# Optimization experiments

Hardware: AMD Instinct MI355X
Metric: run time of the kernel (lower is better)

The kernel has to match this reference:

```python
import jax, jax.numpy as jnp
import numpy as np

N, L, D, H, DFF = 16, 192, 512, 8, 2048
HD = D // H


def _mha(q, k, v, wq, bq, wk, bk, wv, bv, wo, bo, mask=None):
    # q: [B, Lq, D], k/v: [B, Lk, D]
    B, Lq, _ = q.shape
    def proj(x, W, b):
        y = x @ W + b
        return y.reshape(B, -1, H, HD).transpose(0, 2, 1, 3)  # [B, H, L, HD]
    Q, K, V = proj(q, wq, bq), proj(k, wk, bk), proj(v, wv, bv)
    QK = jnp.einsum('bhqd,bhkd->bhqk', Q, K) / jnp.sqrt(jnp.asarray(HD, Q.dtype))
    if mask is not None:
        QK = QK + (1.0 - mask) * (-1e9)
    A = jax.nn.softmax(QK, axis=-1)
    out = jnp.einsum('bhqk,bhkd->bhqd', A, V).transpose(0, 2, 1, 3).reshape(B, Lq, D)
    return out @ wo + bo


def _ln(x, g, b, eps=1e-6):
    mu = x.mean(-1, keepdims=True)
    var = ((x - mu) ** 2).mean(-1, keepdims=True)
    return (x - mu) / jnp.sqrt(var + eps) * g + b


def setup_inputs() -> dict:
    key = jax.random.key(0)
    ks = jax.random.split(key, 16)
    w = lambda k, sh: jax.random.normal(k, sh, jnp.float32) * 0.02
    inp = {
        'S': jax.random.normal(ks[0], (N, L, D), jnp.float32),
        'padding_mask': jax.random.randint(ks[1], (N * N, 1, 1, L), 0, 2, dtype=jnp.int32),
        'training': 0,
    }
    for i, nm in enumerate(['ca_wq', 'ca_wk', 'ca_wv', 'ca_wo', 'ia_wq', 'ia_wk', 'ia_wv', 'ia_wo']):
        inp[nm] = w(ks[2 + i], (D, D))
        inp[nm.replace('w', 'b')] = jnp.zeros((D,), jnp.float32)
    inp['ffn_w1'] = w(ks[10], (D, DFF)); inp['ffn_b1'] = jnp.zeros((DFF,), jnp.float32)
    inp['ffn_w2'] = w(ks[11], (DFF, D)); inp['ffn_b2'] = jnp.zeros((D,), jnp.float32)
    inp['ln1_g'] = jnp.ones((D,), jnp.float32); inp['ln1_b'] = jnp.zeros((D,), jnp.float32)
    inp['ln2_g'] = jnp.ones((D,), jnp.float32); inp['ln2_b'] = jnp.zeros((D,), jnp.float32)
    return inp


def reference(S, ca_wq, ca_bq, ca_wk, ca_bk, ca_wv, ca_bv, ca_wo, ca_bo,
              ia_wq, ia_bq, ia_wk, ia_bk, ia_wv, ia_bv, ia_wo, ia_bo,
              ffn_w1, ffn_b1, ffn_w2, ffn_b2, ln1_g, ln1_b, ln2_g, ln2_b,
              padding_mask, training):
    # training == 0 -> dropout layers are identity (inference mode)
    mask = padding_mask.astype(S.dtype)
    n, l, d = S.shape
    # all-pairs cross attention: query seq i attends to key/value seq j
    queries = jnp.repeat(S, n, axis=0)   # [n*n, l, d]
    keyvalue = jnp.tile(S, (n, 1, 1))    # [n*n, l, d]
    S_attn = _mha(queries, keyvalue, keyvalue,
                  ca_wq, ca_bq, ca_wk, ca_bk, ca_wv, ca_bv, ca_wo, ca_bo, mask=mask)
    S_attn = S_attn.reshape(n, n, l, d).transpose(1, 2, 0, 3).reshape(n * l, n, d)
    S_flip = S.reshape(n * l, 1, d)
    S_attn = _mha(S_flip, S_attn, S_attn,
                  ia_wq, ia_bq, ia_wk, ia_bk, ia_wv, ia_bv, ia_wo, ia_bo)
    S_attn = S_attn.reshape(n, l, d)
    S_norm = _ln(S + S_attn, ln1_g, ln1_b)
    S_ffn = jax.nn.relu(S_norm @ ffn_w1 + ffn_b1) @ ffn_w2 + ffn_b2
    return _ln(S_norm + S_ffn, ln2_g, ln2_b)
```

## Files before the change

kernel.cpp:

```cpp
#include <hip/hip_runtime.h>


using u16 = unsigned short;
using u32 = unsigned int;
typedef __attribute__((ext_vector_type(8))) short short8;
typedef __attribute__((ext_vector_type(4))) float f32x4;

__device__ __forceinline__ u32 cvtpk(float lo, float hi) {
  u32 r;
  asm("v_cvt_pk_bf16_f32 %0, %1, %2" : "=v"(r) : "v"(lo), "v"(hi));
  return r;
}
__device__ __forceinline__ u16 f2bf(float f) { return (u16)cvtpk(f, f); }
__device__ __forceinline__ float bf2f(u16 h) {
  return __uint_as_float(((u32)h) << 16);
}
__device__ __forceinline__ f32x4 mfma16(short8 a, short8 b, f32x4 c) {
  return __builtin_amdgcn_mfma_f32_16x16x32_bf16(a, b, c, 0, 0, 0);
}
__device__ __forceinline__ void gload16(const void* g, u16* l) {
  __builtin_amdgcn_global_load_lds(
      (const __attribute__((address_space(1))) void*)g,
      (__attribute__((address_space(3))) void*)l, 16, 0, 0);
}

template<int ROWS, int NT>
__device__ __forceinline__ void stage_g16(u16* lds, const u16* __restrict__ src,
                                          int ld, int tid) {
  constexpr int UNITS = ROWS * 8;
  constexpr int WV = NT / 64;
  int lane = tid & 63, w = tid >> 6;
  #pragma unroll
  for (int u = 0; u < UNITS / NT; ++u) {
    int base = (u * WV + w) * 64;
    int unit = base + lane;
    int row = unit >> 3, co = unit & 7;
    gload16(src + (long)row * ld + ((co ^ (row & 7)) << 3), lds + base * 8);
  }
}
template<int ROWS, int NT>
__device__ __forceinline__ void stage_f32(u16* lds, const float* __restrict__ src,
                                          int ld, int tid) {
  constexpr int UNITS = ROWS * 8;
  #pragma unroll
  for (int u = 0; u < UNITS / NT; ++u) {
    int unit = tid + u * NT;
    int row = unit >> 3, co = unit & 7;
    const float* g = src + (long)row * ld + (co << 3);
    float4 a = *(const float4*)g;
    float4 b = *(const float4*)(g + 4);
    u32 p[4] = {cvtpk(a.x, a.y), cvtpk(a.z, a.w),
                cvtpk(b.x, b.y), cvtpk(b.z, b.w)};
    *(uint4*)&lds[(row << 6) + ((co ^ (row & 7)) << 3)] = *(const uint4*)p;
  }
}

template<typename AT, typename BT, int BM, int BN, int WM, int WN>
__device__ __forceinline__ void gemm_core(const AT* __restrict__ A, int lda,
                                          const BT* __restrict__ Bt, int ldb, int K,
                                          u16* As, u16* Bs,
                                          f32x4 (&acc)[BM / (WM * 16)][BN / (WN * 16)]) {
  constexpr int NT = WM * WN * 64;
  constexpr int MI = BM / (WM * 16), NJ = BN / (WN * 16);
  int tid = threadIdx.x, lane = tid & 63, wid = tid >> 6;
  int wr = wid % WM, wc = wid / WM;
  int g = lane >> 4, c = lane & 15;
  #pragma unroll
  for (int mi = 0; mi < MI; ++mi)
    #pragma unroll
    for (int nj = 0; nj < NJ; ++nj)
      acc[mi][nj] = f32x4{0.f, 0.f, 0.f, 0.f};
  for (int kb = 0; kb < K; kb += 64) {
    __syncthreads();
    if constexpr (sizeof(AT) == 4) stage_f32<BM, NT>(As, A + kb, lda, tid);
    else                           stage_g16<BM, NT>(As, A + kb, lda, tid);
    if constexpr (sizeof(BT) == 4) stage_f32<BN, NT>(Bs, Bt + kb, ldb, tid);
    else                           stage_g16<BN, NT>(Bs, Bt + kb, ldb, tid);
    __syncthreads();
    #pragma unroll
    for (int kk = 0; kk < 2; ++kk) {
      int sl = ((kk * 4 + g) ^ (c & 7)) << 3;
      short8 af[MI], bfr[NJ];
      #pragma unroll
      for (int mi = 0; mi < MI; ++mi)
        af[mi] = *(const short8*)&As[((wr * (BM / WM) + mi * 16 + c) << 6) + sl];
      #pragma unroll
      for (int nj = 0; nj < NJ; ++nj)
        bfr[nj] = *(const short8*)&Bs[((wc * (BN / WN) + nj * 16 + c) << 6) + sl];
      #pragma unroll
      for (int mi = 0; mi < MI; ++mi)
        #pragma unroll
        for (int nj = 0; nj < NJ; ++nj)
          acc[mi][nj] = mfma16(af[mi], bfr[nj], acc[mi][nj]);
    }
  }
}

struct TJob { const float* src; u16* dst; int R, C, tile0; };
struct TJobs { TJob j[9]; };

__global__ __launch_bounds__(256) void k_transpose(TJobs jobs) {
  __shared__ float tile[32][33];
  int t = blockIdx.x;
  int ji = 0;
  #pragma unroll
  for (int k = 1; k < 9; ++k)
    if (t >= jobs.j[k].tile0) ji = k;
  TJob jb = jobs.j[ji];
  int lt = t - jb.tile0;
  int tpr = jb.C >> 5;
  int tr = lt / tpr, tc = lt % tpr;
  int tid = threadIdx.x;
  #pragma unroll
  for (int u = 0; u < 4; ++u) {
    int e = tid + u * 256;
    int r = e >> 5, cc = e & 31;
    tile[r][cc] = jb.src[(long)(tr * 32 + r) * jb.C + tc * 32 + cc];
  }
  __syncthreads();
  #pragma unroll
  for (int u = 0; u < 4; ++u) {
    int e = tid + u * 256;
    int r = e >> 5, cc = e & 31;
    jb.dst[(long)(tc * 32 + r) * jb.R + tr * 32 + cc] = f2bf(tile[cc][r]);
  }
}

__global__ __launch_bounds__(256) void k_qkv(const float* __restrict__ S,
    const u16* __restrict__ bt0, const u16* __restrict__ bt1,
    const u16* __restrict__ bt2, const u16* __restrict__ bt3,
    const float* __restrict__ b0, const float* __restrict__ b1,
    const float* __restrict__ b2, const float* __restrict__ b3,
    u16* __restrict__ Qc, u16* __restrict__ Kc, u16* __restrict__ Vt,
    u16* __restrict__ Qi) {
  __shared__ u16 As[128 * 64];
  __shared__ u16 Bs[128 * 64];
  int mb = blockIdx.x, nb = blockIdx.y, z = blockIdx.z;
  const u16* bt = z == 0 ? bt0 : z == 1 ? bt1 : z == 2 ? bt2 : bt3;
  const float* bias = z == 0 ? b0 : z == 1 ? b1 : z == 2 ? b2 : b3;
  f32x4 acc[4][4];
  gemm_core<float, u16, 128, 128, 2, 2>(S + (long)mb * 128 * 512, 512,
                                        bt + (long)nb * 128 * 512, 512, 512,
                                        As, Bs, acc);
  int lane = threadIdx.x & 63, wid = threadIdx.x >> 6;
  int wr = wid & 1, wc = wid >> 1, g = lane >> 4, cl = lane & 15;
  #pragma unroll
  for (int mi = 0; mi < 4; ++mi)
    #pragma unroll
    for (int nj = 0; nj < 4; ++nj)
      #pragma unroll
      for (int r = 0; r < 4; ++r) {
        int row = mb * 128 + wr * 64 + mi * 16 + g * 4 + r;
        int col = nb * 128 + wc * 64 + nj * 16 + cl;
        float v = acc[mi][nj][r] + bias[col];
        int seq = row / 192, t = row % 192, h = col >> 6, hd = col & 63;
        if (z == 0)      Qc[((long)(seq * 8 + h) * 192 + t) * 64 + hd] = f2bf(v * 0.125f);
        else if (z == 1) Kc[((long)(seq * 8 + h) * 192 + t) * 64 + hd] = f2bf(v);
        else if (z == 2) Vt[((long)(seq * 8 + h) * 64 + hd) * 192 + t] = f2bf(v);
        else             Qi[(long)row * 512 + col] = f2bf(v * 0.125f);
      }
}

__global__ __launch_bounds__(256) void k_attn_ca(const u16* __restrict__ Qc,
    const u16* __restrict__ Kc, const u16* __restrict__ VtG,
    const int* __restrict__ mask, u16* __restrict__ AC) {
  __shared__ u16 Ks[192 * 64];
  __shared__ u16 Vs[64 * 192];
  __shared__ __align__(16) float mbf[192];
  int bh = blockIdx.x;
  int b = bh >> 3, h = bh & 7;
  int i = b >> 4, j = b & 15;
  int tid = threadIdx.x, lane = tid & 63, w = tid >> 6;
  int g = lane >> 4, c = lane & 15;
  int qb = w * 48;

  const u16* Kbase = Kc + (long)(j * 8 + h) * 192 * 64;
  #pragma unroll
  for (int u = 0; u < 6; ++u) {
    int base = (u * 4 + w) * 64;
    int unit = base + lane;
    int row = unit >> 3, co = unit & 7;
    gload16(Kbase + (long)row * 64 + ((co ^ (row & 7)) << 3), Ks + base * 8);
  }
  const u16* Vbase = VtG + (long)(j * 8 + h) * 64 * 192;
  #pragma unroll
  for (int u = 0; u < 6; ++u) {
    int base = (u * 4 + w) * 64;
    int unit = base + lane;
    int row = unit / 24, co = unit - row * 24;
    gload16(Vbase + (long)row * 192 + ((co ^ (row & 7)) << 3), Vs + base * 8);
  }
  short8 bq[3][2];
  const u16* Qbase = Qc + (long)(i * 8 + h) * 192 * 64;
  #pragma unroll
  for (int nj = 0; nj < 3; ++nj)
    #pragma unroll
    for (int ks = 0; ks < 2; ++ks)
      bq[nj][ks] = *(const short8*)(Qbase + (long)(qb + nj * 16 + c) * 64 + ks * 32 + g * 8);
  if (tid < 192) mbf[tid] = mask[(long)b * 192 + tid] ? 0.f : -1e9f;
  __syncthreads();

  f32x4 oa[4][3];
  #pragma unroll
  for (int mi = 0; mi < 4; ++mi)
    #pragma unroll
    for (int nj = 0; nj < 3; ++nj)
      oa[mi][nj] = f32x4{0.f, 0.f, 0.f, 0.f};
  float sm[3] = {0.f, 0.f, 0.f};
  int srcLo = c | ((g & 1) << 5);
  int srcHi = srcLo + 16;
  int hi = g & 2;

  for (int s = 0; s < 6; ++s) {
    short8 ak[2][2];
    #pragma unroll
    for (int kh = 0; kh < 2; ++kh) {
      int row = (2 * s + kh) * 16 + c;
      #pragma unroll
      for (int ks = 0; ks < 2; ++ks)
        ak[kh][ks] = *(const short8*)&Ks[(row << 6) + (((ks * 4 + g) ^ (c & 7)) << 3)];
    }
    f32x4 sa[2][3];
    __builtin_amdgcn_s_setprio(1);
    #pragma unroll
    for (int kh = 0; kh < 2; ++kh)
      #pragma unroll
      for (int nj = 0; nj < 3; ++nj) {
        sa[kh][nj] = mfma16(ak[kh][0], bq[nj][0], f32x4{0.f, 0.f, 0.f, 0.f});
        sa[kh][nj] = mfma16(ak[kh][1], bq[nj][1], sa[kh][nj]);
      }
    __builtin_amdgcn_s_setprio(0);
    u32 pk[2][3][2];
    #pragma unroll
    for (int kh = 0; kh < 2; ++kh) {
      f32x4 m4 = *(const f32x4*)&mbf[(2 * s + kh) * 16 + g * 4];
      #pragma unroll
      for (int nj = 0; nj < 3; ++nj) {
        float p0 = __expf(sa[kh][nj][0] + m4[0]);
        float p1 = __expf(sa[kh][nj][1] + m4[1]);
        float p2 = __expf(sa[kh][nj][2] + m4[2]);
        float p3 = __expf(sa[kh][nj][3] + m4[3]);
        sm[nj] += (p0 + p1) + (p2 + p3);
        pk[kh][nj][0] = cvtpk(p0, p1);
        pk[kh][nj][1] = cvtpk(p2, p3);
      }
    }
    short8 bfg[3];
    #pragma unroll
    for (int nj = 0; nj < 3; ++nj) {
      u32 w0a = (u32)__shfl((int)pk[0][nj][0], srcLo);
      u32 w0b = (u32)__shfl((int)pk[1][nj][0], srcLo);
      u32 w1a = (u32)__shfl((int)pk[0][nj][1], srcLo);
      u32 w1b = (u32)__shfl((int)pk[1][nj][1], srcLo);
      u32 w2a = (u32)__shfl((int)pk[0][nj][0], srcHi);
      u32 w2b = (u32)__shfl((int)pk[1][nj][0], srcHi);
      u32 w3a = (u32)__shfl((int)pk[0][nj][1], srcHi);
      u32 w3b = (u32)__shfl((int)pk[1][nj][1], srcHi);
      union { u32 u[4]; short8 s8; } bf;
      bf.u[0] = hi ? w0b : w0a;
      bf.u[1] = hi ? w1b : w1a;
      bf.u[2] = hi ? w2b : w2a;
      bf.u[3] = hi ? w3b : w3a;
      bfg[nj] = bf.s8;
    }
    int sl = ((s * 4 + g) ^ (c & 7)) << 3;
    __builtin_amdgcn_s_setprio(1);
    #pragma unroll
    for (int mi = 0; mi < 4; ++mi) {
      short8 av = *(const short8*)&Vs[(mi * 16 + c) * 192 + sl];
      #pragma unroll
      for (int nj = 0; nj < 3; ++nj)
        oa[mi][nj] = mfma16(av, bfg[nj], oa[mi][nj]);
    }
    __builtin_amdgcn_s_setprio(0);
  }
  #pragma unroll
  for (int nj = 0; nj < 3; ++nj) {
    sm[nj] += __shfl_xor(sm[nj], 16);
    sm[nj] += __shfl_xor(sm[nj], 32);
  }
  #pragma unroll
  for (int nj = 0; nj < 3; ++nj) {
    float rs = 1.0f / sm[nj];
    int q = qb + nj * 16 + c;
    u16* dst = AC + ((long)(b * 192 + q)) * 512 + h * 64 + g * 4;
    #pragma unroll
    for (int mi = 0; mi < 4; ++mi) {
      u32 p2[2] = {cvtpk(oa[mi][nj][0] * rs, oa[mi][nj][1] * rs),
                   cvtpk(oa[mi][nj][2] * rs, oa[mi][nj][3] * rs)};
      *(uint2*)(dst + mi * 16) = *(const uint2*)p2;
    }
  }
}

__global__ __launch_bounds__(256) void k_oproj_ca(const u16* __restrict__ AC,
    const u16* __restrict__ woT, const float* __restrict__ bo,
    u16* __restrict__ S2) {
  __shared__ u16 As[128 * 64];
  __shared__ u16 Bs[128 * 64];
  int mb = blockIdx.x, nb = blockIdx.y;
  f32x4 acc[4][4];
  gemm_core<u16, u16, 128, 128, 2, 2>(AC + (long)mb * 128 * 512, 512,
                                      woT + (long)nb * 128 * 512, 512, 512,
                                      As, Bs, acc);
  int lane = threadIdx.x & 63, wid = threadIdx.x >> 6;
  int wr = wid & 1, wc = wid >> 1, g = lane >> 4, cl = lane & 15;
  #pragma unroll
  for (int mi = 0; mi < 4; ++mi)
    #pragma unroll
    for (int nj = 0; nj < 4; ++nj)
      #pragma unroll
      for (int r = 0; r < 4; ++r) {
        int row = mb * 128 + wr * 64 + mi * 16 + g * 4 + r;
        int col = nb * 128 + wc * 64 + nj * 16 + cl;
        int bb = row / 192, t = row % 192;
        int ii = bb >> 4, jj = bb & 15;
        S2[(((long)(jj * 192 + t)) * 16 + ii) * 512 + col] =
            f2bf(acc[mi][nj][r] + bo[col]);
      }
}

__global__ __launch_bounds__(256) void k_uproj(const u16* __restrict__ Qi,
    const float* __restrict__ wk, u16* __restrict__ U) {
  __shared__ u16 As[128 * 64];
  __shared__ u16 Bs[128 * 64];
  int mb = blockIdx.x, nb = blockIdx.y, h = blockIdx.z;
  f32x4 acc[4][4];
  gemm_core<u16, float, 128, 128, 2, 2>(Qi + (long)mb * 128 * 512 + h * 64, 512,
                                        wk + (long)nb * 128 * 512 + h * 64, 512, 64,
                                        As, Bs, acc);
  int lane = threadIdx.x & 63, wid = threadIdx.x >> 6;
  int wr = wid & 1, wc = wid >> 1, g = lane >> 4, cl = lane & 15;
  #pragma unroll
  for (int mi = 0; mi < 4; ++mi)
    #pragma unroll
    for (int nj = 0; nj < 4; ++nj)
      #pragma unroll
      for (int r = 0; r < 4; ++r) {
        int row = mb * 128 + wr * 64 + mi * 16 + g * 4 + r;
        int col = nb * 128 + wc * 64 + nj * 16 + cl;
        U[((long)row * 8 + h) * 512 + col] = f2bf(acc[mi][nj][r]);
      }
}

__global__ __launch_bounds__(256) void k_ia_attn(const u16* __restrict__ S2,
    const u16* __restrict__ U, const u16* __restrict__ Qi,
    const float* __restrict__ bk, u16* __restrict__ Y) {
  __shared__ u16 s2[16 * 520];
  __shared__ float Lp[4][16][17];
  __shared__ float aL[8][16];
  __shared__ float cL[8];
  int tok = blockIdx.x;
  int tid = threadIdx.x, lane = tid & 63, w = tid >> 6;
  {
    const u16* src = S2 + (long)tok * (16 * 512);
    #pragma unroll
    for (int u = 0; u < 4; ++u) {
      int e = tid + u * 256;
      int r = e >> 6, cc = (e & 63) << 3;
      *(uint4*)&s2[r * 520 + cc] = *(const uint4*)(src + r * 512 + cc);
    }
  }
  if (w == 0) {
    int h = lane >> 3, p = lane & 7;
    short8 qv = *(const short8*)(Qi + (long)tok * 512 + h * 64 + p * 8);
    const float* bkp = bk + h * 64 + p * 8;
    float s = 0.f;
    #pragma unroll
    for (int v = 0; v < 8; ++v) s += bf2f((u16)qv[v]) * bkp[v];
    s += __shfl_xor(s, 1); s += __shfl_xor(s, 2); s += __shfl_xor(s, 4);
    if (p == 0) cL[h] = s;
  }
  __syncthreads();
  {
    int g = lane >> 4, c = lane & 15;
    const u16* Ub = U + (long)tok * 4096 + (long)(c & 7) * 512;
    f32x4 accL = {0.f, 0.f, 0.f, 0.f};
    #pragma unroll
    for (int kk = 0; kk < 4; ++kk) {
      int d = w * 128 + kk * 32 + g * 8;
      short8 aS = *(const short8*)&s2[c * 520 + d];
      short8 bU = *(const short8*)(Ub + d);
      accL = mfma16(aS, bU, accL);
    }
    #pragma unroll
    for (int r = 0; r < 4; ++r) Lp[w][g * 4 + r][c] = accL[r];
  }
  __syncthreads();
  if (w == 0) {
    int h = lane & 7, i0 = lane >> 3;
    float L0 = Lp[0][i0][h] + Lp[1][i0][h] + Lp[2][i0][h] + Lp[3][i0][h] + cL[h];
    float L1 = Lp[0][i0 + 8][h] + Lp[1][i0 + 8][h] + Lp[2][i0 + 8][h] +
               Lp[3][i0 + 8][h] + cL[h];
    float e0 = __expf(L0), e1 = __expf(L1);
    float s = e0 + e1;
    s += __shfl_xor(s, 8); s += __shfl_xor(s, 16); s += __shfl_xor(s, 32);
    float rs = 1.0f / s;
    aL[h][i0] = e0 * rs;
    aL[h][i0 + 8] = e1 * rs;
  }
  __syncthreads();
  {
    int h = tid & 7, d0 = (tid >> 3) << 4;
    float y[16];
    #pragma unroll
    for (int v = 0; v < 16; ++v) y[v] = 0.f;
    #pragma unroll
    for (int i = 0; i < 16; ++i) {
      float a = aL[h][i];
      short8 v0 = *(const short8*)&s2[i * 520 + d0];
      short8 v1 = *(const short8*)&s2[i * 520 + d0 + 8];
      #pragma unroll
      for (int v = 0; v < 8; ++v) {
        y[v]     += a * bf2f((u16)v0[v]);
        y[8 + v] += a * bf2f((u16)v1[v]);
      }
    }
    u32 o[8];
    #pragma unroll
    for (int v = 0; v < 8; ++v) o[v] = cvtpk(y[2 * v], y[2 * v + 1]);
    u16* dst = Y + ((long)tok * 8 + h) * 512 + d0;
    *(uint4*)dst = *(const uint4*)&o[0];
    *(uint4*)(dst + 8) = *(const uint4*)&o[4];
  }
}

__global__ __launch_bounds__(256) void k_vapply(const u16* __restrict__ Y,
    const u16* __restrict__ wvT, const float* __restrict__ bv,
    u16* __restrict__ AO) {
  __shared__ u16 As[128 * 64];
  __shared__ u16 Bs[64 * 64];
  int mb = blockIdx.x, h = blockIdx.z;
  f32x4 acc[2][4];
  gemm_core<u16, u16, 128, 64, 4, 1>(Y + (long)mb * 128 * 4096 + h * 512, 4096,
                                     wvT + (long)h * 64 * 512, 512, 512,
                                     As, Bs, acc);
  int lane = threadIdx.x & 63, wid = threadIdx.x >> 6;
  int g = lane >> 4, cl = lane & 15;
  #pragma unroll
  for (int mi = 0; mi < 2; ++mi)
    #pragma unroll
    for (int nj = 0; nj < 4; ++nj)
      #pragma unroll
      for (int r = 0; r < 4; ++r) {
        int row = mb * 128 + wid * 32 + mi * 16 + g * 4 + r;
        int col = h * 64 + nj * 16 + cl;
        AO[(long)row * 512 + col] = f2bf(acc[mi][nj][r] + bv[col]);
      }
}

__global__ __launch_bounds__(256) void k_gemm_f32out(const u16* __restrict__ A, int K,
    const u16* __restrict__ BT, const float* __restrict__ bias,
    float* __restrict__ out) {
  __shared__ u16 As[128 * 64];
  __shared__ u16 Bs[64 * 64];
  int mb = blockIdx.x, nb = blockIdx.y;
  f32x4 acc[4][2];
  gemm_core<u16, u16, 128, 64, 2, 2>(A + (long)mb * 128 * K, K,
                                     BT + (long)nb * 64 * K, K, K, As, Bs, acc);
  int lane = threadIdx.x & 63, wid = threadIdx.x >> 6;
  int wr = wid & 1, wc = wid >> 1, g = lane >> 4, cl = lane & 15;
  #pragma unroll
  for (int mi = 0; mi < 4; ++mi)
    #pragma unroll
    for (int nj = 0; nj < 2; ++nj)
      #pragma unroll
      for (int r = 0; r < 4; ++r) {
        int row = mb * 128 + wr * 64 + mi * 16 + g * 4 + r;
        int col = nb * 64 + wc * 32 + nj * 16 + cl;
        out[(long)row * 512 + col] = acc[mi][nj][r] + bias[col];
      }
}

__global__ __launch_bounds__(256) void k_ffn1(const u16* __restrict__ A,
    const u16* __restrict__ BT, const float* __restrict__ bias,
    u16* __restrict__ out) {
  __shared__ u16 As[128 * 64];
  __shared__ u16 Bs[128 * 64];
  int mb = blockIdx.x, nb = blockIdx.y;
  f32x4 acc[4][4];
  gemm_core<u16, u16, 128, 128, 2, 2>(A + (long)mb * 128 * 512, 512,
                                      BT + (long)nb * 128 * 512, 512, 512,
                                      As, Bs, acc);
  int lane = threadIdx.x & 63, wid = threadIdx.x >> 6;
  int wr = wid & 1, wc = wid >> 1, g = lane >> 4, cl = lane & 15;
  #pragma unroll
  for (int mi = 0; mi < 4; ++mi)
    #pragma unroll
    for (int nj = 0; nj < 4; ++nj)
      #pragma unroll
      for (int r = 0; r < 4; ++r) {
        int row = mb * 128 + wr * 64 + mi * 16 + g * 4 + r;
        int col = nb * 128 + wc * 64 + nj * 16 + cl;
        out[(long)row * 2048 + col] = f2bf(fmaxf(acc[mi][nj][r] + bias[col], 0.f));
      }
}

__global__ __launch_bounds__(256) void k_ln(const float* __restrict__ X1,
    const float* __restrict__ X2, const float* __restrict__ gg,
    const float* __restrict__ bb, float* __restrict__ outF,
    u16* __restrict__ outB) {
  __shared__ float red[8];
  int row = blockIdx.x, tid = threadIdx.x;
  long base = (long)row * 512;
  float x0 = X1[base + tid] + X2[base + tid];
  float x1 = X1[base + tid + 256] + X2[base + tid + 256];
  float s = x0 + x1, ss = x0 * x0 + x1 * x1;
  #pragma unroll
  for (int m = 1; m <= 32; m <<= 1) {
    s += __shfl_xor(s, m);
    ss += __shfl_xor(ss, m);
  }
  int w = tid >> 6;
  if ((tid & 63) == 0) { red[w] = s; red[4 + w] = ss; }
  __syncthreads();
  s = red[0] + red[1] + red[2] + red[3];
  ss = red[4] + red[5] + red[6] + red[7];
  float mu = s * (1.0f / 512.0f);
  float var = ss * (1.0f / 512.0f) - mu * mu;
  float rstd = 1.0f / sqrtf(var + 1e-6f);
  float y0 = (x0 - mu) * rstd * gg[tid] + bb[tid];
  float y1 = (x1 - mu) * rstd * gg[tid + 256] + bb[tid + 256];
  if (outF) { outF[base + tid] = y0; outF[base + tid + 256] = y1; }
  if (outB) { outB[base + tid] = f2bf(y0); outB[base + tid + 256] = f2bf(y1); }
}

extern "C" void kernel_launch(void* const* d_in, const int* in_sizes, int n_in,
                              void* d_out, int out_size, void* d_ws, size_t ws_size,
                              hipStream_t stream) {
  const float* S      = (const float*)d_in[0];
  const int*   maskp  = (const int*)d_in[1];
  const float* ca_wq  = (const float*)d_in[3];
  const float* ca_bq  = (const float*)d_in[4];
  const float* ca_wk  = (const float*)d_in[5];
  const float* ca_bk  = (const float*)d_in[6];
  const float* ca_wv  = (const float*)d_in[7];
  const float* ca_bv  = (const float*)d_in[8];
  const float* ca_wo  = (const float*)d_in[9];
  const float* ca_bo  = (const float*)d_in[10];
  const float* ia_wq  = (const float*)d_in[11];
  const float* ia_bq  = (const float*)d_in[12];
  const float* ia_wk  = (const float*)d_in[13];
  const float* ia_bk  = (const float*)d_in[14];
  const float* ia_wv  = (const float*)d_in[15];
  const float* ia_bv  = (const float*)d_in[16];
  const float* ia_wo  = (const float*)d_in[17];
  const float* ia_bo  = (const float*)d_in[18];
  const float* ffn_w1 = (const float*)d_in[19];
  const float* ffn_b1 = (const float*)d_in[20];
  const float* ffn_w2 = (const float*)d_in[21];
  const float* ffn_b2 = (const float*)d_in[22];
  const float* ln1_g  = (const float*)d_in[23];
  const float* ln1_b  = (const float*)d_in[24];
  const float* ln2_g  = (const float*)d_in[25];
  const float* ln2_b  = (const float*)d_in[26];

  char* ws = (char*)d_ws;
  constexpr size_t OFF_WQT  = 0;
  constexpr size_t OFF_WKT  = 524288;
  constexpr size_t OFF_WVT  = 1048576;
  constexpr size_t OFF_IQT  = 1572864;
  constexpr size_t OFF_WOTC = 2097152;
  constexpr size_t OFF_WVTI = 2621440;
  constexpr size_t OFF_WOTI = 3145728;
  constexpr size_t OFF_W1T  = 3670016;
  constexpr size_t OFF_W2T  = 5767168;
  constexpr size_t OFF_QC   = 7864320;
  constexpr size_t OFF_KC   = 11010048;
  constexpr size_t OFF_VT   = 14155776;
  constexpr size_t OFF_QI   = 17301504;
  constexpr size_t OFF_AC   = 20447232;
  constexpr size_t OFF_S2   = 70778880;
  constexpr size_t OFF_U    = OFF_AC;
  constexpr size_t OFF_Y    = OFF_AC + 25165824;
  constexpr size_t OFF_AO   = OFF_QI;
  constexpr size_t OFF_IAO  = OFF_QC;
  constexpr size_t OFF_SNB  = OFF_VT;
  constexpr size_t OFF_SNF  = OFF_S2;
  constexpr size_t OFF_HFF  = OFF_S2 + 6291456;
  constexpr size_t OFF_FFO  = OFF_HFF + 12582912;

  u16* wqT  = (u16*)(ws + OFF_WQT);
  u16* wkT  = (u16*)(ws + OFF_WKT);
  u16* wvT  = (u16*)(ws + OFF_WVT);
  u16* iqT  = (u16*)(ws + OFF_IQT);
  u16* woTc = (u16*)(ws + OFF_WOTC);
  u16* wvTi = (u16*)(ws + OFF_WVTI);
  u16* woTi = (u16*)(ws + OFF_WOTI);
  u16* w1T  = (u16*)(ws + OFF_W1T);
  u16* w2T  = (u16*)(ws + OFF_W2T);
  u16* Qc   = (u16*)(ws + OFF_QC);
  u16* Kc   = (u16*)(ws + OFF_KC);
  u16* Vt   = (u16*)(ws + OFF_VT);
  u16* Qi   = (u16*)(ws + OFF_QI);
  u16* AC   = (u16*)(ws + OFF_AC);
  u16* S2   = (u16*)(ws + OFF_S2);
  u16* U    = (u16*)(ws + OFF_U);
  u16* Y    = (u16*)(ws + OFF_Y);
  u16* AO   = (u16*)(ws + OFF_AO);
  float* IAO = (float*)(ws + OFF_IAO);
  u16* SNB  = (u16*)(ws + OFF_SNB);
  float* SNF = (float*)(ws + OFF_SNF);
  u16* HFF  = (u16*)(ws + OFF_HFF);
  float* FFO = (float*)(ws + OFF_FFO);

  TJobs tj;
  int t0 = 0;
  auto SET = [&](int k, const float* s, u16* d, int R, int C) {
    tj.j[k].src = s; tj.j[k].dst = d; tj.j[k].R = R; tj.j[k].C = C; tj.j[k].tile0 = t0;
    t0 += (R / 32) * (C / 32);
  };
  SET(0, ca_wq, wqT, 512, 512);
  SET(1, ca_wk, wkT, 512, 512);
  SET(2, ca_wv, wvT, 512, 512);
  SET(3, ia_wq, iqT, 512, 512);
  SET(4, ca_wo, woTc, 512, 512);
  SET(5, ia_wv, wvTi, 512, 512);
  SET(6, ia_wo, woTi, 512, 512);
  SET(7, ffn_w1, w1T, 512, 2048);
  SET(8, ffn_w2, w2T, 2048, 512);

  k_transpose<<<dim3(t0), 256, 0, stream>>>(tj);
  k_qkv<<<dim3(24, 4, 4), 256, 0, stream>>>(S, wqT, wkT, wvT, iqT,
                                            ca_bq, ca_bk, ca_bv, ia_bq,
                                            Qc, Kc, Vt, Qi);
  k_attn_ca<<<dim3(2048), 256, 0, stream>>>(Qc, Kc, Vt, maskp, AC);
  k_oproj_ca<<<dim3(384, 4), 256, 0, stream>>>(AC, woTc, ca_bo, S2);
  k_uproj<<<dim3(24, 4, 8), 256, 0, stream>>>(Qi, ia_wk, U);
  k_ia_attn<<<dim3(3072), 256, 0, stream>>>(S2, U, Qi, ia_bk, Y);
  k_vapply<<<dim3(24, 1, 8), 256, 0, stream>>>(Y, wvTi, ia_bv, AO);
  k_gemm_f32out<<<dim3(24, 8), 256, 0, stream>>>(AO, 512, woTi, ia_bo, IAO);
  k_ln<<<dim3(3072), 256, 0, stream>>>(S, IAO, ln1_g, ln1_b, SNF, SNB);
  k_ffn1<<<dim3(24, 16), 256, 0, stream>>>(SNB, w1T, ffn_b1, HFF);
  k_gemm_f32out<<<dim3(24, 8), 256, 0, stream>>>(HFF, 2048, w2T, ffn_b2, FFO);
  k_ln<<<dim3(3072), 256, 0, stream>>>(SNF, FFO, ln2_g, ln2_b, (float*)d_out, nullptr);
}
```

Before: 214.2 us.

## Swizzle GEMM block order across XCDs and write S2 contiguously

New measurement: 210.8 us. Within noise of the previous version (-1.6%).

```diff
diff --git a/kernel.cpp b/kernel.cpp
--- a/kernel.cpp
+++ b/kernel.cpp
@@ -135,7 +135,9 @@
     u16* __restrict__ Qi) {
   __shared__ u16 As[128 * 64];
   __shared__ u16 Bs[128 * 64];
-  int mb = blockIdx.x, nb = blockIdx.y, z = blockIdx.z;
+  int f = blockIdx.x;
+  int swz = (f & 7) * 12 + (f >> 3);
+  int mb = swz >> 2, nb = swz & 3, z = blockIdx.y;
   const u16* bt = z == 0 ? bt0 : z == 1 ? bt1 : z == 2 ? bt2 : bt3;
   const float* bias = z == 0 ? b0 : z == 1 ? b1 : z == 2 ? b2 : b3;
   f32x4 acc[4][4];
@@ -298,7 +300,9 @@
     u16* __restrict__ S2) {
   __shared__ u16 As[128 * 64];
   __shared__ u16 Bs[128 * 64];
-  int mb = blockIdx.x, nb = blockIdx.y;
+  int f = blockIdx.x;
+  int swz = (f & 7) * 192 + (f >> 3);
+  int mb = swz >> 2, nb = swz & 3;
   f32x4 acc[4][4];
   gemm_core<u16, u16, 128, 128, 2, 2>(AC + (long)mb * 128 * 512, 512,
                                       woT + (long)nb * 128 * 512, 512, 512,
@@ -313,10 +317,7 @@
       for (int r = 0; r < 4; ++r) {
         int row = mb * 128 + wr * 64 + mi * 16 + g * 4 + r;
         int col = nb * 128 + wc * 64 + nj * 16 + cl;
-        int bb = row / 192, t = row % 192;
-        int ii = bb >> 4, jj = bb & 15;
-        S2[(((long)(jj * 192 + t)) * 16 + ii) * 512 + col] =
-            f2bf(acc[mi][nj][r] + bo[col]);
+        S2[(long)row * 512 + col] = f2bf(acc[mi][nj][r] + bo[col]);
       }
 }
 
@@ -353,12 +354,12 @@
   int tok = blockIdx.x;
   int tid = threadIdx.x, lane = tid & 63, w = tid >> 6;
   {
-    const u16* src = S2 + (long)tok * (16 * 512);
+    const u16* src = S2 + (long)tok * 512;
     #pragma unroll
     for (int u = 0; u < 4; ++u) {
       int e = tid + u * 256;
       int r = e >> 6, cc = (e & 63) << 3;
-      *(uint4*)&s2[r * 520 + cc] = *(const uint4*)(src + r * 512 + cc);
+      *(uint4*)&s2[r * 520 + cc] = *(const uint4*)(src + (long)r * 3072 * 512 + cc);
     }
   }
   if (w == 0) {
@@ -454,7 +455,9 @@
     float* __restrict__ out) {
   __shared__ u16 As[128 * 64];
   __shared__ u16 Bs[64 * 64];
-  int mb = blockIdx.x, nb = blockIdx.y;
+  int f = blockIdx.x;
+  int swz = (f & 7) * 24 + (f >> 3);
+  int mb = swz >> 3, nb = swz & 7;
   f32x4 acc[4][2];
   gemm_core<u16, u16, 128, 64, 2, 2>(A + (long)mb * 128 * K, K,
                                      BT + (long)nb * 64 * K, K, K, As, Bs, acc);
@@ -477,7 +480,9 @@
     u16* __restrict__ out) {
   __shared__ u16 As[128 * 64];
   __shared__ u16 Bs[128 * 64];
-  int mb = blockIdx.x, nb = blockIdx.y;
+  int f = blockIdx.x;
+  int swz = (f & 7) * 48 + (f >> 3);
+  int mb = swz >> 4, nb = swz & 15;
   f32x4 acc[4][4];
   gemm_core<u16, u16, 128, 128, 2, 2>(A + (long)mb * 128 * 512, 512,
                                       BT + (long)nb * 128 * 512, 512, 512,
@@ -621,17 +626,17 @@
   SET(8, ffn_w2, w2T, 2048, 512);
 
   k_transpose<<<dim3(t0), 256, 0, stream>>>(tj);
-  k_qkv<<<dim3(24, 4, 4), 256, 0, stream>>>(S, wqT, wkT, wvT, iqT,
-                                            ca_bq, ca_bk, ca_bv, ia_bq,
-                                            Qc, Kc, Vt, Qi);
+  k_qkv<<<dim3(96, 4), 256, 0, stream>>>(S, wqT, wkT, wvT, iqT,
+                                         ca_bq, ca_bk, ca_bv, ia_bq,
+                                         Qc, Kc, Vt, Qi);
   k_attn_ca<<<dim3(2048), 256, 0, stream>>>(Qc, Kc, Vt, maskp, AC);
-  k_oproj_ca<<<dim3(384, 4), 256, 0, stream>>>(AC, woTc, ca_bo, S2);
+  k_oproj_ca<<<dim3(1536), 256, 0, stream>>>(AC, woTc, ca_bo, S2);
   k_uproj<<<dim3(24, 4, 8), 256, 0, stream>>>(Qi, ia_wk, U);
   k_ia_attn<<<dim3(3072), 256, 0, stream>>>(S2, U, Qi, ia_bk, Y);
   k_vapply<<<dim3(24, 1, 8), 256, 0, stream>>>(Y, wvTi, ia_bv, AO);
-  k_gemm_f32out<<<dim3(24, 8), 256, 0, stream>>>(AO, 512, woTi, ia_bo, IAO);
+  k_gemm_f32out<<<dim3(192), 256, 0, stream>>>(AO, 512, woTi, ia_bo, IAO);
   k_ln<<<dim3(3072), 256, 0, stream>>>(S, IAO, ln1_g, ln1_b, SNF, SNB);
-  k_ffn1<<<dim3(24, 16), 256, 0, stream>>>(SNB, w1T, ffn_b1, HFF);
-  k_gemm_f32out<<<dim3(24, 8), 256, 0, stream>>>(HFF, 2048, w2T, ffn_b2, FFO);
+  k_ffn1<<<dim3(384), 256, 0, stream>>>(SNB, w1T, ffn_b1, HFF);
+  k_gemm_f32out<<<dim3(192), 256, 0, stream>>>(HFF, 2048, w2T, ffn_b2, FFO);
   k_ln<<<dim3(3072), 256, 0, stream>>>(SNF, FFO, ln2_g, ln2_b, (float*)d_out, nullptr);
 }
```
